# Kernel tuning notes

Hardware: AMD Instinct MI355X
Metric: run time of the kernel (lower is better)

The kernel has to match this reference:

```python
import jax, jax.numpy as jnp
import numpy as np

B, T, F, U, M, OUT = 2048, 16, 512, 512, 8, 3
DELTA_T = 0.04
EPS = 1e-07


def setup_inputs() -> dict:
    key = jax.random.key(0)
    ks = jax.random.split(key, 6)
    s_in = 1.0 / np.sqrt(F + U)
    s_u = 1.0 / np.sqrt(U)
    return {
        "x": jax.random.normal(ks[0], (B, T, F), dtype=jnp.float32),
        "W_r": jax.random.normal(ks[1], (F + U, U * M), dtype=jnp.float32) * s_in,
        "b_r": jnp.zeros((U * M,), dtype=jnp.float32),
        "W_q": jax.random.normal(ks[2], (F + U, U), dtype=jnp.float32) * s_in,
        "b_q": jnp.zeros((U,), dtype=jnp.float32),
        "W_s": jax.random.normal(ks[3], (F + U, U * M), dtype=jnp.float32) * s_in,
        "b_s": jnp.zeros((U * M,), dtype=jnp.float32),
        "W_o": jax.random.normal(ks[4], (U, OUT), dtype=jnp.float32) * s_u,
        "b_o": jnp.zeros((OUT,), dtype=jnp.float32),
    }


def _ln_tau_table():
    # tau_i = 10^(i/2)  =>  ln tau_i = i * 0.5 * ln(10)
    return (jnp.arange(M, dtype=jnp.float32) * (0.5 * np.log(10.0)))


def reference(x, W_r, b_r, W_q, b_q, W_s, b_s, W_o, b_o):
    ln_tau = _ln_tau_table()                       # (M,)
    decay = jnp.exp(-DELTA_T / (jnp.exp(ln_tau) + EPS))  # (M,)

    def step(h_hat, x_t):
        # h_hat: (B, U, M), x_t: (B, F)
        h = h_hat.sum(axis=2)                       # (B, U)
        fi = jnp.concatenate([x_t, h], axis=1)      # (B, F+U)
        ln_r = (fi @ W_r + b_r).reshape(-1, U, M)
        r = jax.nn.softmax(-jnp.square(ln_r - ln_tau), axis=2)
        ctx = jnp.sum(r * h_hat, axis=2)            # (B, U)
        q = jnp.tanh(jnp.concatenate([x_t, ctx], axis=1) @ W_q + b_q)[:, :, None]
        ln_s = (fi @ W_s + b_s).reshape(-1, U, M)
        s = jax.nn.softmax(-jnp.square(ln_s - ln_tau), axis=2)
        h_hat_next = ((1.0 - s) * h_hat + s * q) * decay
        hidden = h_hat_next.sum(axis=2)             # (B, U)
        return h_hat_next, hidden

    h0 = jnp.zeros((x.shape[0], U, M), dtype=x.dtype)
    xs = jnp.swapaxes(x, 0, 1)                      # (T, B, F)
    _, hs = jax.lax.scan(step, h0, xs)              # hs: (T, B, U)
    hs = jnp.swapaxes(hs, 0, 1)                     # (B, T, U)
    out = hs @ W_o + b_o                            # (B, T, OUT)
    return out
```

## Files before the change

kernel.cpp:

```cpp
#include <hip/hip_runtime.h>
#include <math.h>

#define B_ 2048
#define T_ 16
#define F_ 512
#define U_ 512
#define M_ 8

typedef _Float16 half8 __attribute__((ext_vector_type(8)));
typedef float f32x4 __attribute__((ext_vector_type(4)));

__device__ __forceinline__ void load_lds16(const _Float16* gsrc, _Float16* lds) {
    __builtin_amdgcn_global_load_lds(
        (const __attribute__((address_space(1))) void*)gsrc,
        (__attribute__((address_space(3))) void*)lds, 16, 0, 0);
}

#define BAR() __builtin_amdgcn_s_barrier()
#define LGKM0() asm volatile("s_waitcnt lgkmcnt(0)" ::: "memory")
#define VMW(n) asm volatile("s_waitcnt vmcnt(" #n ")" ::: "memory")
#define MFMA16(a, b, c) __builtin_amdgcn_mfma_f32_16x16x32_f16(a, b, c, 0, 0, 0)

struct Decay8 { float d[8]; };

__global__ __launch_bounds__(256) void cast_x_kernel(const float* __restrict__ in,
                                                     _Float16* __restrict__ out) {
    long i = (long)blockIdx.x * 256 + threadIdx.x;
    const f32x4* p = (const f32x4*)in;
    f32x4 a = p[i * 2], b = p[i * 2 + 1];
    half8 v;
    v[0] = (_Float16)a[0]; v[1] = (_Float16)a[1]; v[2] = (_Float16)a[2]; v[3] = (_Float16)a[3];
    v[4] = (_Float16)b[0]; v[5] = (_Float16)b[1]; v[6] = (_Float16)b[2]; v[7] = (_Float16)b[3];
    ((half8*)out)[i] = v;
}

__global__ __launch_bounds__(256) void transpose_cast_kernel(const float* __restrict__ W,
                                                             _Float16* __restrict__ Wt,
                                                             int K, int N) {
    __shared__ float tile[32][33];
    int n0 = blockIdx.x * 32, k0 = blockIdx.y * 32;
    int tx = threadIdx.x, ty = threadIdx.y;
    #pragma unroll
    for (int i = 0; i < 32; i += 8)
        tile[ty + i][tx] = W[(long)(k0 + ty + i) * N + n0 + tx];
    __syncthreads();
    #pragma unroll
    for (int i = 0; i < 32; i += 8)
        Wt[(long)(n0 + ty + i) * K + k0 + tx] = (_Float16)tile[tx][ty + i];
}

__global__ __launch_bounds__(256) void transpose_cast_perm_kernel(const float* __restrict__ W,
                                                                  _Float16* __restrict__ Wt,
                                                                  int rowbase) {
    const int K = 1024, N = 4096;
    __shared__ float tile[32][33];
    int n0 = blockIdx.x * 32, k0 = blockIdx.y * 32;
    int tx = threadIdx.x, ty = threadIdx.y;
    #pragma unroll
    for (int i = 0; i < 32; i += 8)
        tile[ty + i][tx] = W[(long)(k0 + ty + i) * N + n0 + tx];
    __syncthreads();
    #pragma unroll
    for (int i = 0; i < 32; i += 8) {
        int nl = n0 + ty + i;
        int u = nl >> 3, m = nl & 7;
        int nn = ((u >> 4) << 7) + (m << 4) + (u & 15);
        Wt[(long)(rowbase + nn) * K + k0 + tx] = (_Float16)tile[tx][ty + i];
    }
}

__global__ __launch_bounds__(512, 2) void gemm1_fused_kernel(
    const _Float16* __restrict__ A0, long lda0,
    const _Float16* __restrict__ A1, long lda1,
    const _Float16* __restrict__ Wt,
    const float* __restrict__ b_r, const float* __restrict__ b_s,
    const _Float16* __restrict__ h_hat,
    _Float16* __restrict__ ctx,
    _Float16* __restrict__ s_buf,
    int nt) {
    const float LT = 1.1512925464970228f;
    __shared__ __align__(16) _Float16 As[2][256 * 64];
    __shared__ __align__(16) _Float16 Bs[2][256 * 64];
    const int tid = threadIdx.x;
    const int lane = tid & 63;
    const int wave = tid >> 6;
    const int wm = wave >> 1, wn = wave & 1;
    const int l15 = lane & 15, lhi = lane >> 4, swz = lane & 7;
    const int g0 = (lhi ^ swz) * 8;
    const int g1 = ((lhi + 4) ^ swz) * 8;
    const int srow = tid >> 3;
    const int sg = (tid & 7) ^ (srow & 7);
    const int ldsdst = wave * 64 * 8;
    const long m0 = (long)blockIdx.y * 256;
    const long n0 = (long)blockIdx.x * 256;

#define STAGE_A(kt_, buf_, r_) do {                                             \
        int kt__ = (kt_);                                                       \
        const _Float16* s_; long lda_; int kofs_;                               \
        if (kt__ < 8) { s_ = A0; lda_ = lda0; kofs_ = kt__ * 64; }              \
        else          { s_ = A1; lda_ = lda1; kofs_ = kt__ * 64 - 512; }        \
        load_lds16(s_ + (m0 + (r_) * 64 + srow) * lda_ + kofs_ + sg * 8,        \
                   &As[buf_][(r_) * 4096 + ldsdst]);                            \
    } while (0)
#define STAGE_B(kt_, buf_, r_)                                                  \
        load_lds16(Wt + (n0 + (r_) * 64 + srow) * 1024 + (kt_) * 64 + sg * 8,   \
                   &Bs[buf_][(r_) * 4096 + ldsdst])

    f32x4 acc[4][8] = {};

    #pragma unroll
    for (int r = 0; r < 4; ++r) STAGE_A(0, 0, r);
    #pragma unroll
    for (int r = 0; r < 4; ++r) STAGE_B(0, 0, r);
    #pragma unroll
    for (int r = 0; r < 4; ++r) STAGE_A(1, 1, r);
    STAGE_B(1, 1, 0); STAGE_B(1, 1, 2);
    VMW(6);
    BAR();

    #pragma unroll 1
    for (int t = 0; t < nt; ++t) {
        const int cur = t & 1, nxt = cur ^ 1;
        const _Float16* Ac = &As[cur][0];
        const _Float16* Bc = &Bs[cur][0];
        half8 af[4][2], bfa[2][2], bfb[2][2];

        #pragma unroll
        for (int i = 0; i < 4; ++i) {
            const _Float16* p = Ac + (wm * 64 + i * 16 + l15) * 64;
            af[i][0] = *(const half8*)(p + g0);
            af[i][1] = *(const half8*)(p + g1);
        }
        #pragma unroll
        for (int j = 0; j < 2; ++j) {
            const _Float16* p = Bc + (wn * 128 + j * 16 + l15) * 64;
            bfa[j][0] = *(const half8*)(p + g0);
            bfa[j][1] = *(const half8*)(p + g1);
        }
        if (t + 1 < nt) { STAGE_B(t + 1, nxt, 1); STAGE_B(t + 1, nxt, 3); }
        LGKM0();
        __builtin_amdgcn_s_setprio(1);
        #pragma unroll
        for (int i = 0; i < 4; ++i)
            #pragma unroll
            for (int j = 0; j < 2; ++j) {
                acc[i][j] = MFMA16(af[i][0], bfa[j][0], acc[i][j]);
                acc[i][j] = MFMA16(af[i][1], bfa[j][1], acc[i][j]);
            }
        __builtin_amdgcn_s_setprio(0);
        BAR();

        #pragma unroll
        for (int j = 0; j < 2; ++j) {
            const _Float16* p = Bc + (wn * 128 + (2 + j) * 16 + l15) * 64;
            bfb[j][0] = *(const half8*)(p + g0);
            bfb[j][1] = *(const half8*)(p + g1);
        }
        if (t + 2 < nt) { STAGE_A(t + 2, cur, 0); STAGE_A(t + 2, cur, 1); }
        BAR(); LGKM0();
        __builtin_amdgcn_s_setprio(1);
        #pragma unroll
        for (int i = 0; i < 4; ++i)
            #pragma unroll
            for (int j = 0; j < 2; ++j) {
                acc[i][2 + j] = MFMA16(af[i][0], bfb[j][0], acc[i][2 + j]);
                acc[i][2 + j] = MFMA16(af[i][1], bfb[j][1], acc[i][2 + j]);
            }
        __builtin_amdgcn_s_setprio(0);
        BAR();

        #pragma unroll
        for (int j = 0; j < 2; ++j) {
            const _Float16* p = Bc + (wn * 128 + (4 + j) * 16 + l15) * 64;
            bfa[j][0] = *(const half8*)(p + g0);
            bfa[j][1] = *(const half8*)(p + g1);
        }
        if (t + 2 < nt) { STAGE_A(t + 2, cur, 2); STAGE_A(t + 2, cur, 3); }
        LGKM0();
        __builtin_amdgcn_s_setprio(1);
        #pragma unroll
        for (int i = 0; i < 4; ++i)
            #pragma unroll
            for (int j = 0; j < 2; ++j) {
                acc[i][4 + j] = MFMA16(af[i][0], bfa[j][0], acc[i][4 + j]);
                acc[i][4 + j] = MFMA16(af[i][1], bfa[j][1], acc[i][4 + j]);
            }
        __builtin_amdgcn_s_setprio(0);
        BAR();

        #pragma unroll
        for (int j = 0; j < 2; ++j) {
            const _Float16* p = Bc + (wn * 128 + (6 + j) * 16 + l15) * 64;
            bfb[j][0] = *(const half8*)(p + g0);
            bfb[j][1] = *(const half8*)(p + g1);
        }
        if (t + 2 < nt) { STAGE_B(t + 2, cur, 0); STAGE_B(t + 2, cur, 2); }
        LGKM0();
        __builtin_amdgcn_s_setprio(1);
        #pragma unroll
        for (int i = 0; i < 4; ++i)
            #pragma unroll
            for (int j = 0; j < 2; ++j) {
                acc[i][6 + j] = MFMA16(af[i][0], bfb[j][0], acc[i][6 + j]);
                acc[i][6 + j] = MFMA16(af[i][1], bfb[j][1], acc[i][6 + j]);
            }
        __builtin_amdgcn_s_setprio(0);
        if (t + 2 < nt)      { VMW(6); }
        else if (t + 1 < nt) { VMW(0); }
        BAR();
    }

    const int r4 = lhi * 4;
    const int panel = (int)(n0 >> 7) + wn;
    const bool is_r = panel < 32;
    const int u = (is_r ? panel : panel - 32) * 16 + l15;
    const float* bias = is_r ? b_r : b_s;
    f32x4 bl0 = *(const f32x4*)(bias + u * 8);
    f32x4 bl1 = *(const f32x4*)(bias + u * 8 + 4);

    #pragma unroll
    for (int i = 0; i < 4; ++i) {
        #pragma unroll
        for (int r = 0; r < 4; ++r) {
            long m = m0 + wm * 64 + i * 16 + r4 + r;
            float z[8]; float zmax = -1e30f;
            #pragma unroll
            for (int j = 0; j < 8; ++j) {
                float v = acc[i][j][r] + (j < 4 ? bl0[j] : bl1[j - 4]);
                float d = v - (float)j * LT;
                z[j] = -d * d;
                zmax = fmaxf(zmax, z[j]);
            }
            float e[8]; float se = 0.f;
            #pragma unroll
            for (int j = 0; j < 8; ++j) { e[j] = __expf(z[j] - zmax); se += e[j]; }
            float inv = 1.f / se;
            if (is_r) {
                half8 hh = *(const half8*)(h_hat + m * 4096 + u * 8);
                float c = 0.f;
                #pragma unroll
                for (int j = 0; j < 8; ++j) c += e[j] * (float)hh[j];
                ctx[m * 512 + u] = (_Float16)(c * inv);
            } else {
                half8 sv;
                #pragma unroll
                for (int j = 0; j < 8; ++j) sv[j] = (_Float16)(e[j] * inv);
                *(half8*)(s_buf + m * 4096 + u * 8) = sv;
            }
        }
    }
#undef STAGE_A
#undef STAGE_B
}

__global__ __launch_bounds__(512) void gemm2_fused_kernel(
    const _Float16* __restrict__ A0, long lda0,
    const _Float16* __restrict__ A1, long lda1,
    const _Float16* __restrict__ Wt,
    const float* __restrict__ bias,
    const _Float16* __restrict__ s_buf,
    _Float16* __restrict__ h_hat,
    _Float16* __restrict__ hs_t,
    Decay8 dec, int nt) {
    __shared__ __align__(16) _Float16 As[2][64 * 64];
    __shared__ __align__(16) _Float16 Bs[2][64 * 64];
    const int tid = threadIdx.x;
    const int lane = tid & 63;
    const int wave = tid >> 6;
    const int wm = wave >> 1, wn = wave & 1;
    const int l15 = lane & 15, lhi = lane >> 4, swz = lane & 7;
    const int g0 = (lhi ^ swz) * 8;
    const int g1 = ((lhi + 4) ^ swz) * 8;
    const int srow = tid >> 3;
    const int sg = (tid & 7) ^ (srow & 7);
    const long m0 = (long)blockIdx.y * 64;
    const long n0 = (long)blockIdx.x * 64;

#define STAGE2(kt_, buf_) do {                                                  \
        int kt__ = (kt_);                                                       \
        const _Float16* s_; long lda_; int kofs_;                               \
        if (kt__ < 8) { s_ = A0; lda_ = lda0; kofs_ = kt__ * 64; }              \
        else          { s_ = A1; lda_ = lda1; kofs_ = kt__ * 64 - 512; }        \
        load_lds16(s_ + (m0 + srow) * lda_ + kofs_ + sg * 8,                    \
                   &As[buf_][wave * 512]);                                      \
        load_lds16(Wt + (n0 + srow) * 1024 + kt__ * 64 + sg * 8,                \
                   &Bs[buf_][wave * 512]);                                      \
    } while (0)

    f32x4 acc[2] = {};

    STAGE2(0, 0);
    #pragma unroll 1
    for (int kt = 0; kt < nt; ++kt) {
        const int cur = kt & 1;
        if (kt + 1 < nt) { STAGE2(kt + 1, cur ^ 1); VMW(2); }
        else             { VMW(0); }
        BAR();
        const _Float16* Ac = &As[cur][0];
        const _Float16* Bc = &Bs[cur][0];
        half8 af[2], bf[2][2];
        {
            const _Float16* p = Ac + (wm * 16 + l15) * 64;
            af[0] = *(const half8*)(p + g0);
            af[1] = *(const half8*)(p + g1);
        }
        #pragma unroll
        for (int j = 0; j < 2; ++j) {
            const _Float16* p = Bc + (wn * 32 + j * 16 + l15) * 64;
            bf[j][0] = *(const half8*)(p + g0);
            bf[j][1] = *(const half8*)(p + g1);
        }
        LGKM0();
        #pragma unroll
        for (int j = 0; j < 2; ++j) {
            acc[j] = MFMA16(af[0], bf[j][0], acc[j]);
            acc[j] = MFMA16(af[1], bf[j][1], acc[j]);
        }
        BAR();
    }
#undef STAGE2

    const int r4 = lhi * 4;
    const int c16 = lane & 15;
    #pragma unroll
    for (int j = 0; j < 2; ++j) {
        #pragma unroll
        for (int r = 0; r < 4; ++r) {
            long b = m0 + wm * 16 + r4 + r;
            long u = n0 + wn * 32 + j * 16 + c16;
            float q = tanhf(acc[j][r] + bias[u]);
            half8 s8 = *(const half8*)(s_buf + b * 4096 + u * 8);
            half8 h8 = *(const half8*)(h_hat + b * 4096 + u * 8);
            half8 hn;
            float hval = 0.f;
            #pragma unroll
            for (int m = 0; m < 8; ++m) {
                float sm = (float)s8[m];
                float x = ((1.f - sm) * (float)h8[m] + sm * q) * dec.d[m];
                hn[m] = (_Float16)x;
                hval += x;
            }
            *(half8*)(h_hat + b * 4096 + u * 8) = hn;
            hs_t[b * 512 + u] = (_Float16)hval;
        }
    }
}

__global__ __launch_bounds__(64) void out_proj_kernel(const _Float16* __restrict__ hs,
                                                      const float* __restrict__ W_o,
                                                      const float* __restrict__ b_o,
                                                      float* __restrict__ out) {
    const int bt = blockIdx.x;
    const int t = bt >> 11, b = bt & 2047;
    const int lane = threadIdx.x;
    half8 v = *(const half8*)(hs + ((long)t * 2048 + b) * 512 + lane * 8);
    float p0 = 0.f, p1 = 0.f, p2 = 0.f;
    #pragma unroll
    for (int m = 0; m < 8; ++m) {
        float hv = (float)v[m];
        int u = lane * 8 + m;
        p0 += hv * W_o[u * 3 + 0];
        p1 += hv * W_o[u * 3 + 1];
        p2 += hv * W_o[u * 3 + 2];
    }
    #pragma unroll
    for (int s = 32; s > 0; s >>= 1) {
        p0 += __shfl_down(p0, s);
        p1 += __shfl_down(p1, s);
        p2 += __shfl_down(p2, s);
    }
    if (lane == 0) {
        long o = ((long)b * T_ + t) * 3;
        out[o + 0] = p0 + b_o[0];
        out[o + 1] = p1 + b_o[1];
        out[o + 2] = p2 + b_o[2];
    }
}

extern "C" void kernel_launch(void* const* d_in, const int* in_sizes, int n_in,
                              void* d_out, int out_size, void* d_ws, size_t ws_size,
                              hipStream_t stream) {
    const float* x   = (const float*)d_in[0];
    const float* W_r = (const float*)d_in[1];
    const float* b_r = (const float*)d_in[2];
    const float* W_q = (const float*)d_in[3];
    const float* b_q = (const float*)d_in[4];
    const float* W_s = (const float*)d_in[5];
    const float* b_s = (const float*)d_in[6];
    const float* W_o = (const float*)d_in[7];
    const float* b_o = (const float*)d_in[8];
    float* out = (float*)d_out;

    char* ws = (char*)d_ws;
    size_t off = 0;
    _Float16* x_h   = (_Float16*)(ws + off); off += (size_t)B_ * T_ * F_ * 2;
    _Float16* Wrs_t = (_Float16*)(ws + off); off += (size_t)8192 * 1024 * 2;
    _Float16* Wq_t  = (_Float16*)(ws + off); off += (size_t)512 * 1024 * 2;
    _Float16* s_buf = (_Float16*)(ws + off); off += (size_t)B_ * 4096 * 2;
    _Float16* h_hat = (_Float16*)(ws + off); off += (size_t)B_ * 4096 * 2;
    _Float16* ctx_h = (_Float16*)(ws + off); off += (size_t)B_ * U_ * 2;
    _Float16* hs    = (_Float16*)(ws + off); off += (size_t)T_ * B_ * U_ * 2;
    _Float16* zbuf  = (_Float16*)(ws + off); off += (size_t)B_ * U_ * 2;
    if (ws_size < off) return;

    hipMemsetAsync(h_hat, 0, (size_t)B_ * 4096 * 2, stream);
    hipMemsetAsync(zbuf, 0, (size_t)B_ * U_ * 2, stream);

    cast_x_kernel<<<dim3((B_ * T_ * F_) / (256 * 8)), 256, 0, stream>>>(x, x_h);
    transpose_cast_perm_kernel<<<dim3(4096 / 32, 1024 / 32), dim3(32, 8), 0, stream>>>(W_r, Wrs_t, 0);
    transpose_cast_perm_kernel<<<dim3(4096 / 32, 1024 / 32), dim3(32, 8), 0, stream>>>(W_s, Wrs_t, 4096);
    transpose_cast_kernel<<<dim3(512 / 32, 1024 / 32), dim3(32, 8), 0, stream>>>(W_q, Wq_t, 1024, 512);

    Decay8 dec;
    for (int m = 0; m < 8; ++m) {
        float lt = (float)m * 1.1512925464970228f;
        dec.d[m] = expf(-0.04f / (expf(lt) + 1e-7f));
    }

    for (int t = 0; t < T_; ++t) {
        const _Float16* hprev = (t == 0) ? zbuf : hs + (size_t)(t - 1) * B_ * U_;
        const int nt = (t == 0) ? 8 : 16;
        gemm1_fused_kernel<<<dim3(8192 / 256, B_ / 256), 512, 0, stream>>>(
            x_h + (long)t * F_, (long)T_ * F_, hprev, U_, Wrs_t,
            b_r, b_s, h_hat, ctx_h, s_buf, nt);
        gemm2_fused_kernel<<<dim3(512 / 64, B_ / 64), 512, 0, stream>>>(
            x_h + (long)t * F_, (long)T_ * F_, ctx_h, U_, Wq_t,
            b_q, s_buf, h_hat, hs + (size_t)t * B_ * U_, dec, nt);
    }
    out_proj_kernel<<<dim3(B_ * T_), 64, 0, stream>>>(hs, W_o, b_o, out);
    (void)in_sizes; (void)n_in; (void)out_size;
}
```

Baseline: 988.6 us.

## Fuse recurrent timestep loop into one persistent cooperative kernel with grid syncs

Replaces the 32 per-timestep launches of the two GEMM kernels with one cooperative persistent kernel of 256 blocks that loops over all timesteps and uses grid.sync between phases. At t=0 it skips the blocks whose output depends only on the zero hidden state (r-gate half) and removes the zero buffer, and it prefetches the next step's x and weight tiles into LDS before the grid barrier. The intent is to remove launch overhead and inter-kernel gaps. The cost is one block per CU with a 128KB LDS footprint, a small 256-block grid for the second GEMM, and grid-wide barrier latency.

```diff
diff --git a/kernel.cpp b/kernel.cpp
--- a/kernel.cpp
+++ b/kernel.cpp
@@ -1,5 +1,8 @@
 #include <hip/hip_runtime.h>
+#include <hip/hip_cooperative_groups.h>
 #include <math.h>
+
+namespace cg = cooperative_groups;
 
 #define B_ 2048
 #define T_ 16
@@ -69,18 +72,24 @@
     }
 }
 
-__global__ __launch_bounds__(512, 2) void gemm1_fused_kernel(
-    const _Float16* __restrict__ A0, long lda0,
-    const _Float16* __restrict__ A1, long lda1,
-    const _Float16* __restrict__ Wt,
+__global__ __launch_bounds__(512, 1) void ctgru_mega(
+    const _Float16* __restrict__ x_all,
+    const _Float16* __restrict__ Wrs,
+    const _Float16* __restrict__ Wq,
     const float* __restrict__ b_r, const float* __restrict__ b_s,
-    const _Float16* __restrict__ h_hat,
+    const float* __restrict__ b_q,
+    _Float16* __restrict__ h_hat,
     _Float16* __restrict__ ctx,
     _Float16* __restrict__ s_buf,
-    int nt) {
+    _Float16* __restrict__ hs,
+    Decay8 dec) {
+    cg::grid_group grid = cg::this_grid();
     const float LT = 1.1512925464970228f;
-    __shared__ __align__(16) _Float16 As[2][256 * 64];
-    __shared__ __align__(16) _Float16 Bs[2][256 * 64];
+    __shared__ __align__(16) _Float16 lds[65536];
+#define AS(b_) (lds + (b_) * 16384)
+#define BS(b_) (lds + 32768 + (b_) * 16384)
+#define A2(b_) (lds + 49152 + (b_) * 4096)
+#define B2(b_) (lds + 57344 + (b_) * 4096)
     const int tid = threadIdx.x;
     const int lane = tid & 63;
     const int wave = tid >> 6;
@@ -90,260 +99,275 @@
     const int g1 = ((lhi + 4) ^ swz) * 8;
     const int srow = tid >> 3;
     const int sg = (tid & 7) ^ (srow & 7);
-    const int ldsdst = wave * 64 * 8;
-    const long m0 = (long)blockIdx.y * 256;
-    const long n0 = (long)blockIdx.x * 256;
-
-#define STAGE_A(kt_, buf_, r_) do {                                             \
-        int kt__ = (kt_);                                                       \
-        const _Float16* s_; long lda_; int kofs_;                               \
-        if (kt__ < 8) { s_ = A0; lda_ = lda0; kofs_ = kt__ * 64; }              \
-        else          { s_ = A1; lda_ = lda1; kofs_ = kt__ * 64 - 512; }        \
-        load_lds16(s_ + (m0 + (r_) * 64 + srow) * lda_ + kofs_ + sg * 8,        \
-                   &As[buf_][(r_) * 4096 + ldsdst]);                            \
+    const int ldsdst = wave * 512;
+    const int bid = blockIdx.x;
+    const int bx = bid & 31, by = bid >> 5;
+    const long m1 = (long)by * 256, n1 = (long)bx * 256;
+    const int gx = bid & 7, gy = bid >> 3;
+    const long m2 = (long)gy * 64, n2 = (long)gx * 64;
+    const long ldax = (long)T_ * F_;
+
+#define STG1_A(kt_, buf_, r_) do {                                              \
+        int kk_ = (kt_);                                                        \
+        const _Float16* s_; long lda_; int ko_;                                 \
+        if (kk_ < 8) { s_ = A0; lda_ = ldax; ko_ = kk_ * 64; }                  \
+        else         { s_ = A1; lda_ = 512;  ko_ = kk_ * 64 - 512; }            \
+        load_lds16(s_ + (m1 + (r_) * 64 + srow) * lda_ + ko_ + sg * 8,          \
+                   AS(buf_) + (r_) * 4096 + ldsdst);                            \
     } while (0)
-#define STAGE_B(kt_, buf_, r_)                                                  \
-        load_lds16(Wt + (n0 + (r_) * 64 + srow) * 1024 + (kt_) * 64 + sg * 8,   \
-                   &Bs[buf_][(r_) * 4096 + ldsdst])
-
-    f32x4 acc[4][8] = {};
-
-    #pragma unroll
-    for (int r = 0; r < 4; ++r) STAGE_A(0, 0, r);
-    #pragma unroll
-    for (int r = 0; r < 4; ++r) STAGE_B(0, 0, r);
-    #pragma unroll
-    for (int r = 0; r < 4; ++r) STAGE_A(1, 1, r);
-    STAGE_B(1, 1, 0); STAGE_B(1, 1, 2);
-    VMW(6);
-    BAR();
+#define STG1_B(kt_, buf_, r_)                                                   \
+        load_lds16(Wrs + (n1 + (r_) * 64 + srow) * 1024 + (kt_) * 64 + sg * 8,  \
+                   BS(buf_) + (r_) * 4096 + ldsdst)
 
     #pragma unroll 1
-    for (int t = 0; t < nt; ++t) {
-        const int cur = t & 1, nxt = cur ^ 1;
-        const _Float16* Ac = &As[cur][0];
-        const _Float16* Bc = &Bs[cur][0];
-        half8 af[4][2], bfa[2][2], bfb[2][2];
-
-        #pragma unroll
-        for (int i = 0; i < 4; ++i) {
-            const _Float16* p = Ac + (wm * 64 + i * 16 + l15) * 64;
-            af[i][0] = *(const half8*)(p + g0);
-            af[i][1] = *(const half8*)(p + g1);
+    for (int t = 0; t < T_; ++t) {
+        const int nt = (t == 0) ? 8 : 16;
+        const _Float16* A0 = x_all + (long)t * F_;
+        const _Float16* A1 = hs + (size_t)(t - 1) * B_ * U_;
+        const bool act = (t > 0) || (bx >= 16);
+
+        if (act) {
+            if (t == 0) {
+                #pragma unroll
+                for (int r = 0; r < 4; ++r) STG1_A(0, 0, r);
+                #pragma unroll
+                for (int r = 0; r < 4; ++r) STG1_B(0, 0, r);
+                #pragma unroll
+                for (int r = 0; r < 4; ++r) STG1_A(1, 1, r);
+                STG1_B(1, 1, 0); STG1_B(1, 1, 2);
+            } else {
+                STG1_B(1, 1, 0); STG1_B(1, 1, 2);
+            }
+            VMW(6);
+            BAR();
+
+            f32x4 acc[4][8] = {};
+            #pragma unroll 1
+            for (int it = 0; it < nt; ++it) {
+                const int cur = it & 1, nxt = cur ^ 1;
+                const _Float16* Ac = AS(cur);
+                const _Float16* Bc = BS(cur);
+                half8 af[4][2], bfa[2][2], bfb[2][2];
+
+                #pragma unroll
+                for (int i = 0; i < 4; ++i) {
+                    const _Float16* p = Ac + (wm * 64 + i * 16 + l15) * 64;
+                    af[i][0] = *(const half8*)(p + g0);
+                    af[i][1] = *(const half8*)(p + g1);
+                }
+                #pragma unroll
+                for (int j = 0; j < 2; ++j) {
+                    const _Float16* p = Bc + (wn * 128 + j * 16 + l15) * 64;
+                    bfa[j][0] = *(const half8*)(p + g0);
+                    bfa[j][1] = *(const half8*)(p + g1);
+                }
+                if (it + 1 < nt) { STG1_B(it + 1, nxt, 1); STG1_B(it + 1, nxt, 3); }
+                LGKM0();
+                __builtin_amdgcn_s_setprio(1);
+                #pragma unroll
+                for (int i = 0; i < 4; ++i)
+                    #pragma unroll
+                    for (int j = 0; j < 2; ++j) {
+                        acc[i][j] = MFMA16(af[i][0], bfa[j][0], acc[i][j]);
+                        acc[i][j] = MFMA16(af[i][1], bfa[j][1], acc[i][j]);
+                    }
+                __builtin_amdgcn_s_setprio(0);
+                BAR();
+
+                #pragma unroll
+                for (int j = 0; j < 2; ++j) {
+                    const _Float16* p = Bc + (wn * 128 + (2 + j) * 16 + l15) * 64;
+                    bfb[j][0] = *(const half8*)(p + g0);
+                    bfb[j][1] = *(const half8*)(p + g1);
+                }
+                if (it + 2 < nt) { STG1_A(it + 2, cur, 0); STG1_A(it + 2, cur, 1); }
+                BAR(); LGKM0();
+                __builtin_amdgcn_s_setprio(1);
+                #pragma unroll
+                for (int i = 0; i < 4; ++i)
+                    #pragma unroll
+                    for (int j = 0; j < 2; ++j) {
+                        acc[i][2 + j] = MFMA16(af[i][0], bfb[j][0], acc[i][2 + j]);
+                        acc[i][2 + j] = MFMA16(af[i][1], bfb[j][1], acc[i][2 + j]);
+                    }
+                __builtin_amdgcn_s_setprio(0);
+                BAR();
+
+                #pragma unroll
+                for (int j = 0; j < 2; ++j) {
+                    const _Float16* p = Bc + (wn * 128 + (4 + j) * 16 + l15) * 64;
+                    bfa[j][0] = *(const half8*)(p + g0);
+                    bfa[j][1] = *(const half8*)(p + g1);
+                }
+                if (it + 2 < nt) { STG1_A(it + 2, cur, 2); STG1_A(it + 2, cur, 3); }
+                LGKM0();
+                __builtin_amdgcn_s_setprio(1);
+                #pragma unroll
+                for (int i = 0; i < 4; ++i)
+                    #pragma unroll
+                    for (int j = 0; j < 2; ++j) {
+                        acc[i][4 + j] = MFMA16(af[i][0], bfa[j][0], acc[i][4 + j]);
+                        acc[i][4 + j] = MFMA16(af[i][1], bfa[j][1], acc[i][4 + j]);
+                    }
+                __builtin_amdgcn_s_setprio(0);
+                BAR();
+
+                #pragma unroll
+                for (int j = 0; j < 2; ++j) {
+                    const _Float16* p = Bc + (wn * 128 + (6 + j) * 16 + l15) * 64;
+                    bfb[j][0] = *(const half8*)(p + g0);
+                    bfb[j][1] = *(const half8*)(p + g1);
+                }
+                if (it + 2 < nt) { STG1_B(it + 2, cur, 0); STG1_B(it + 2, cur, 2); }
+                LGKM0();
+                __builtin_amdgcn_s_setprio(1);
+                #pragma unroll
+                for (int i = 0; i < 4; ++i)
+                    #pragma unroll
+                    for (int j = 0; j < 2; ++j) {
+                        acc[i][6 + j] = MFMA16(af[i][0], bfb[j][0], acc[i][6 + j]);
+                        acc[i][6 + j] = MFMA16(af[i][1], bfb[j][1], acc[i][6 + j]);
+                    }
+                __builtin_amdgcn_s_setprio(0);
+                if (it + 2 < nt)      { VMW(6); }
+                else if (it + 1 < nt) { VMW(0); }
+                BAR();
+            }
+
+            const int r4 = lhi * 4;
+            const int panel = (int)(n1 >> 7) + wn;
+            const bool is_r = panel < 32;
+            const int u = (is_r ? panel : panel - 32) * 16 + l15;
+            const float* bias = is_r ? b_r : b_s;
+            f32x4 bl0 = *(const f32x4*)(bias + u * 8);
+            f32x4 bl1 = *(const f32x4*)(bias + u * 8 + 4);
+            #pragma unroll
+            for (int i = 0; i < 4; ++i) {
+                #pragma unroll
+                for (int r = 0; r < 4; ++r) {
+                    long m = m1 + wm * 64 + i * 16 + r4 + r;
+                    float z[8]; float zmax = -1e30f;
+                    #pragma unroll
+                    for (int j = 0; j < 8; ++j) {
+                        float v = acc[i][j][r] + (j < 4 ? bl0[j] : bl1[j - 4]);
+                        float d = v - (float)j * LT;
+                        z[j] = -d * d;
+                        zmax = fmaxf(zmax, z[j]);
+                    }
+                    float e[8]; float se = 0.f;
+                    #pragma unroll
+                    for (int j = 0; j < 8; ++j) { e[j] = __expf(z[j] - zmax); se += e[j]; }
+                    float inv = 1.f / se;
+                    if (is_r) {
+                        half8 hh = *(const half8*)(h_hat + m * 4096 + u * 8);
+                        float c = 0.f;
+                        #pragma unroll
+                        for (int j = 0; j < 8; ++j) c += e[j] * (float)hh[j];
+                        ctx[m * 512 + u] = (_Float16)(c * inv);
+                    } else {
+                        half8 sv;
+                        #pragma unroll
+                        for (int j = 0; j < 8; ++j) sv[j] = (_Float16)(e[j] * inv);
+                        *(half8*)(s_buf + m * 4096 + u * 8) = sv;
+                    }
+                }
+            }
         }
-        #pragma unroll
-        for (int j = 0; j < 2; ++j) {
-            const _Float16* p = Bc + (wn * 128 + j * 16 + l15) * 64;
-            bfa[j][0] = *(const half8*)(p + g0);
-            bfa[j][1] = *(const half8*)(p + g1);
-        }
-        if (t + 1 < nt) { STAGE_B(t + 1, nxt, 1); STAGE_B(t + 1, nxt, 3); }
-        LGKM0();
-        __builtin_amdgcn_s_setprio(1);
-        #pragma unroll
-        for (int i = 0; i < 4; ++i)
+        grid.sync();
+
+        {
+            _Float16* hs_t = hs + (size_t)t * B_ * U_;
+#define STG2(kt_, buf_) do {                                                    \
+            int kk_ = (kt_);                                                    \
+            const _Float16* s_; long lda_; int ko_;                             \
+            if (kk_ < 8) { s_ = A0;  lda_ = ldax; ko_ = kk_ * 64; }             \
+            else         { s_ = ctx; lda_ = 512;  ko_ = kk_ * 64 - 512; }       \
+            load_lds16(s_ + (m2 + srow) * lda_ + ko_ + sg * 8,                  \
+                       A2(buf_) + wave * 512);                                  \
+            load_lds16(Wq + (n2 + srow) * 1024 + kk_ * 64 + sg * 8,             \
+                       B2(buf_) + wave * 512);                                  \
+        } while (0)
+
+            f32x4 acc2[2] = {};
+            STG2(0, 0);
+            #pragma unroll 1
+            for (int kt = 0; kt < nt; ++kt) {
+                const int cur = kt & 1;
+                if (kt + 1 < nt) { STG2(kt + 1, cur ^ 1); VMW(2); }
+                else             { VMW(0); }
+                BAR();
+                const _Float16* Ac = A2(cur);
+                const _Float16* Bc = B2(cur);
+                half8 af[2], bf[2][2];
+                {
+                    const _Float16* p = Ac + (wm * 16 + l15) * 64;
+                    af[0] = *(const half8*)(p + g0);
+                    af[1] = *(const half8*)(p + g1);
+                }
+                #pragma unroll
+                for (int j = 0; j < 2; ++j) {
+                    const _Float16* p = Bc + (wn * 32 + j * 16 + l15) * 64;
+                    bf[j][0] = *(const half8*)(p + g0);
+                    bf[j][1] = *(const half8*)(p + g1);
+                }
+                LGKM0();
+                #pragma unroll
+                for (int j = 0; j < 2; ++j) {
+                    acc2[j] = MFMA16(af[0], bf[j][0], acc2[j]);
+                    acc2[j] = MFMA16(af[1], bf[j][1], acc2[j]);
+                }
+                BAR();
+            }
+#undef STG2
+
+            const int r4 = lhi * 4;
             #pragma unroll
             for (int j = 0; j < 2; ++j) {
-                acc[i][j] = MFMA16(af[i][0], bfa[j][0], acc[i][j]);
-                acc[i][j] = MFMA16(af[i][1], bfa[j][1], acc[i][j]);
-            }
-        __builtin_amdgcn_s_setprio(0);
-        BAR();
-
-        #pragma unroll
-        for (int j = 0; j < 2; ++j) {
-            const _Float16* p = Bc + (wn * 128 + (2 + j) * 16 + l15) * 64;
-            bfb[j][0] = *(const half8*)(p + g0);
-            bfb[j][1] = *(const half8*)(p + g1);
-        }
-        if (t + 2 < nt) { STAGE_A(t + 2, cur, 0); STAGE_A(t + 2, cur, 1); }
-        BAR(); LGKM0();
-        __builtin_amdgcn_s_setprio(1);
-        #pragma unroll
-        for (int i = 0; i < 4; ++i)
-            #pragma unroll
-            for (int j = 0; j < 2; ++j) {
-                acc[i][2 + j] = MFMA16(af[i][0], bfb[j][0], acc[i][2 + j]);
-                acc[i][2 + j] = MFMA16(af[i][1], bfb[j][1], acc[i][2 + j]);
-            }
-        __builtin_amdgcn_s_setprio(0);
-        BAR();
-
-        #pragma unroll
-        for (int j = 0; j < 2; ++j) {
-            const _Float16* p = Bc + (wn * 128 + (4 + j) * 16 + l15) * 64;
-            bfa[j][0] = *(const half8*)(p + g0);
-            bfa[j][1] = *(const half8*)(p + g1);
-        }
-        if (t + 2 < nt) { STAGE_A(t + 2, cur, 2); STAGE_A(t + 2, cur, 3); }
-        LGKM0();
-        __builtin_amdgcn_s_setprio(1);
-        #pragma unroll
-        for (int i = 0; i < 4; ++i)
-            #pragma unroll
-            for (int j = 0; j < 2; ++j) {
-                acc[i][4 + j] = MFMA16(af[i][0], bfa[j][0], acc[i][4 + j]);
-                acc[i][4 + j] = MFMA16(af[i][1], bfa[j][1], acc[i][4 + j]);
-            }
-        __builtin_amdgcn_s_setprio(0);
-        BAR();
-
-        #pragma unroll
-        for (int j = 0; j < 2; ++j) {
-            const _Float16* p = Bc + (wn * 128 + (6 + j) * 16 + l15) * 64;
-            bfb[j][0] = *(const half8*)(p + g0);
-            bfb[j][1] = *(const half8*)(p + g1);
-        }
-        if (t + 2 < nt) { STAGE_B(t + 2, cur, 0); STAGE_B(t + 2, cur, 2); }
-        LGKM0();
-        __builtin_amdgcn_s_setprio(1);
-        #pragma unroll
-        for (int i = 0; i < 4; ++i)
-            #pragma unroll
-            for (int j = 0; j < 2; ++j) {
-                acc[i][6 + j] = MFMA16(af[i][0], bfb[j][0], acc[i][6 + j]);
-                acc[i][6 + j] = MFMA16(af[i][1], bfb[j][1], acc[i][6 + j]);
-            }
-        __builtin_amdgcn_s_setprio(0);
-        if (t + 2 < nt)      { VMW(6); }
-        else if (t + 1 < nt) { VMW(0); }
-        BAR();
-    }
-
-    const int r4 = lhi * 4;
-    const int panel = (int)(n0 >> 7) + wn;
-    const bool is_r = panel < 32;
-    const int u = (is_r ? panel : panel - 32) * 16 + l15;
-    const float* bias = is_r ? b_r : b_s;
-    f32x4 bl0 = *(const f32x4*)(bias + u * 8);
-    f32x4 bl1 = *(const f32x4*)(bias + u * 8 + 4);
-
-    #pragma unroll
-    for (int i = 0; i < 4; ++i) {
-        #pragma unroll
-        for (int r = 0; r < 4; ++r) {
-            long m = m0 + wm * 64 + i * 16 + r4 + r;
-            float z[8]; float zmax = -1e30f;
-            #pragma unroll
-            for (int j = 0; j < 8; ++j) {
-                float v = acc[i][j][r] + (j < 4 ? bl0[j] : bl1[j - 4]);
-                float d = v - (float)j * LT;
-                z[j] = -d * d;
-                zmax = fmaxf(zmax, z[j]);
-            }
-            float e[8]; float se = 0.f;
-            #pragma unroll
-            for (int j = 0; j < 8; ++j) { e[j] = __expf(z[j] - zmax); se += e[j]; }
-            float inv = 1.f / se;
-            if (is_r) {
-                half8 hh = *(const half8*)(h_hat + m * 4096 + u * 8);
-                float c = 0.f;
-                #pragma unroll
-                for (int j = 0; j < 8; ++j) c += e[j] * (float)hh[j];
-                ctx[m * 512 + u] = (_Float16)(c * inv);
-            } else {
-                half8 sv;
-                #pragma unroll
-                for (int j = 0; j < 8; ++j) sv[j] = (_Float16)(e[j] * inv);
-                *(half8*)(s_buf + m * 4096 + u * 8) = sv;
+                #pragma unroll
+                for (int r = 0; r < 4; ++r) {
+                    long b = m2 + wm * 16 + r4 + r;
+                    long u = n2 + wn * 32 + j * 16 + l15;
+                    float q = tanhf(acc2[j][r] + b_q[u]);
+                    half8 s8 = *(const half8*)(s_buf + b * 4096 + u * 8);
+                    half8 h8 = *(const half8*)(h_hat + b * 4096 + u * 8);
+                    half8 hn;
+                    float hval = 0.f;
+                    #pragma unroll
+                    for (int m = 0; m < 8; ++m) {
+                        float sm = (float)s8[m];
+                        float x = ((1.f - sm) * (float)h8[m] + sm * q) * dec.d[m];
+                        hn[m] = (_Float16)x;
+                        hval += x;
+                    }
+                    *(half8*)(h_hat + b * 4096 + u * 8) = hn;
+                    hs_t[b * 512 + u] = (_Float16)hval;
+                }
             }
         }
-    }
-#undef STAGE_A
-#undef STAGE_B
-}
-
-__global__ __launch_bounds__(512) void gemm2_fused_kernel(
-    const _Float16* __restrict__ A0, long lda0,
-    const _Float16* __restrict__ A1, long lda1,
-    const _Float16* __restrict__ Wt,
-    const float* __restrict__ bias,
-    const _Float16* __restrict__ s_buf,
-    _Float16* __restrict__ h_hat,
-    _Float16* __restrict__ hs_t,
-    Decay8 dec, int nt) {
-    __shared__ __align__(16) _Float16 As[2][64 * 64];
-    __shared__ __align__(16) _Float16 Bs[2][64 * 64];
-    const int tid = threadIdx.x;
-    const int lane = tid & 63;
-    const int wave = tid >> 6;
-    const int wm = wave >> 1, wn = wave & 1;
-    const int l15 = lane & 15, lhi = lane >> 4, swz = lane & 7;
-    const int g0 = (lhi ^ swz) * 8;
-    const int g1 = ((lhi + 4) ^ swz) * 8;
-    const int srow = tid >> 3;
-    const int sg = (tid & 7) ^ (srow & 7);
-    const long m0 = (long)blockIdx.y * 64;
-    const long n0 = (long)blockIdx.x * 64;
-
-#define STAGE2(kt_, buf_) do {                                                  \
-        int kt__ = (kt_);                                                       \
-        const _Float16* s_; long lda_; int kofs_;                               \
-        if (kt__ < 8) { s_ = A0; lda_ = lda0; kofs_ = kt__ * 64; }              \
-        else          { s_ = A1; lda_ = lda1; kofs_ = kt__ * 64 - 512; }        \
-        load_lds16(s_ + (m0 + srow) * lda_ + kofs_ + sg * 8,                    \
-                   &As[buf_][wave * 512]);                                      \
-        load_lds16(Wt + (n0 + srow) * 1024 + kt__ * 64 + sg * 8,                \
-                   &Bs[buf_][wave * 512]);                                      \
-    } while (0)
-
-    f32x4 acc[2] = {};
-
-    STAGE2(0, 0);
-    #pragma unroll 1
-    for (int kt = 0; kt < nt; ++kt) {
-        const int cur = kt & 1;
-        if (kt + 1 < nt) { STAGE2(kt + 1, cur ^ 1); VMW(2); }
-        else             { VMW(0); }
-        BAR();
-        const _Float16* Ac = &As[cur][0];
-        const _Float16* Bc = &Bs[cur][0];
-        half8 af[2], bf[2][2];
-        {
-            const _Float16* p = Ac + (wm * 16 + l15) * 64;
-            af[0] = *(const half8*)(p + g0);
-            af[1] = *(const half8*)(p + g1);
+
+        if (t + 1 < T_) {
+            const _Float16* A0n = x_all + (long)(t + 1) * F_;
+            #pragma unroll
+            for (int r = 0; r < 4; ++r)
+                load_lds16(A0n + (m1 + r * 64 + srow) * ldax + sg * 8,
+                           AS(0) + r * 4096 + ldsdst);
+            #pragma unroll
+            for (int r = 0; r < 4; ++r)
+                load_lds16(Wrs + (n1 + r * 64 + srow) * 1024 + sg * 8,
+                           BS(0) + r * 4096 + ldsdst);
+            #pragma unroll
+            for (int r = 0; r < 4; ++r)
+                load_lds16(A0n + (m1 + r * 64 + srow) * ldax + 64 + sg * 8,
+                           AS(1) + r * 4096 + ldsdst);
+            grid.sync();
         }
-        #pragma unroll
-        for (int j = 0; j < 2; ++j) {
-            const _Float16* p = Bc + (wn * 32 + j * 16 + l15) * 64;
-            bf[j][0] = *(const half8*)(p + g0);
-            bf[j][1] = *(const half8*)(p + g1);
-        }
-        LGKM0();
-        #pragma unroll
-        for (int j = 0; j < 2; ++j) {
-            acc[j] = MFMA16(af[0], bf[j][0], acc[j]);
-            acc[j] = MFMA16(af[1], bf[j][1], acc[j]);
-        }
-        BAR();
-    }
-#undef STAGE2
-
-    const int r4 = lhi * 4;
-    const int c16 = lane & 15;
-    #pragma unroll
-    for (int j = 0; j < 2; ++j) {
-        #pragma unroll
-        for (int r = 0; r < 4; ++r) {
-            long b = m0 + wm * 16 + r4 + r;
-            long u = n0 + wn * 32 + j * 16 + c16;
-            float q = tanhf(acc[j][r] + bias[u]);
-            half8 s8 = *(const half8*)(s_buf + b * 4096 + u * 8);
-            half8 h8 = *(const half8*)(h_hat + b * 4096 + u * 8);
-            half8 hn;
-            float hval = 0.f;
-            #pragma unroll
-            for (int m = 0; m < 8; ++m) {
-                float sm = (float)s8[m];
-                float x = ((1.f - sm) * (float)h8[m] + sm * q) * dec.d[m];
-                hn[m] = (_Float16)x;
-                hval += x;
-            }
-            *(half8*)(h_hat + b * 4096 + u * 8) = hn;
-            hs_t[b * 512 + u] = (_Float16)hval;
-        }
-    }
+    }
+#undef STG1_A
+#undef STG1_B
+#undef AS
+#undef BS
+#undef A2
+#undef B2
 }
 
 __global__ __launch_bounds__(64) void out_proj_kernel(const _Float16* __restrict__ hs,
@@ -400,11 +424,9 @@
     _Float16* h_hat = (_Float16*)(ws + off); off += (size_t)B_ * 4096 * 2;
     _Float16* ctx_h = (_Float16*)(ws + off); off += (size_t)B_ * U_ * 2;
     _Float16* hs    = (_Float16*)(ws + off); off += (size_t)T_ * B_ * U_ * 2;
-    _Float16* zbuf  = (_Float16*)(ws + off); off += (size_t)B_ * U_ * 2;
     if (ws_size < off) return;
 
     hipMemsetAsync(h_hat, 0, (size_t)B_ * 4096 * 2, stream);
-    hipMemsetAsync(zbuf, 0, (size_t)B_ * U_ * 2, stream);
 
     cast_x_kernel<<<dim3((B_ * T_ * F_) / (256 * 8)), 256, 0, stream>>>(x, x_h);
     transpose_cast_perm_kernel<<<dim3(4096 / 32, 1024 / 32), dim3(32, 8), 0, stream>>>(W_r, Wrs_t, 0);
@@ -417,16 +439,13 @@
         dec.d[m] = expf(-0.04f / (expf(lt) + 1e-7f));
     }
 
-    for (int t = 0; t < T_; ++t) {
-        const _Float16* hprev = (t == 0) ? zbuf : hs + (size_t)(t - 1) * B_ * U_;
-        const int nt = (t == 0) ? 8 : 16;
-        gemm1_fused_kernel<<<dim3(8192 / 256, B_ / 256), 512, 0, stream>>>(
-            x_h + (long)t * F_, (long)T_ * F_, hprev, U_, Wrs_t,
-            b_r, b_s, h_hat, ctx_h, s_buf, nt);
-        gemm2_fused_kernel<<<dim3(512 / 64, B_ / 64), 512, 0, stream>>>(
-            x_h + (long)t * F_, (long)T_ * F_, ctx_h, U_, Wq_t,
-            b_q, s_buf, h_hat, hs + (size_t)t * B_ * U_, dec, nt);
-    }
+    void* kargs[] = {(void*)&x_h, (void*)&Wrs_t, (void*)&Wq_t,
+                     (void*)&b_r, (void*)&b_s, (void*)&b_q,
+                     (void*)&h_hat, (void*)&ctx_h, (void*)&s_buf, (void*)&hs,
+                     (void*)&dec};
+    hipLaunchCooperativeKernel((void*)ctgru_mega, dim3(256), dim3(512),
+                               kargs, 0, stream);
+
     out_proj_kernel<<<dim3(B_ * T_), 64, 0, stream>>>(hs, W_o, b_o, out);
     (void)in_sizes; (void)n_in; (void)out_size;
 }
```

Result: slower. 1.977 ms (+100.0%).
